# Optimization experiments

Measured on AMD Instinct MI355X. Metric: run time of the kernel, lower is better.

The kernel has to match this reference:

```python
import jax, jax.numpy as jnp
import numpy as np
import math

B, S, D, H, FF, NB = 32, 512, 512, 8, 2048, 2
DK = D // H  # 64
NEG = -1e30  # stands in for torch's -1e32 (fp32-safe)


def _make_pe():
    # CosinePositionalEmbedding: deterministic sin/cos part (the 0.1*randn is fully overwritten)
    pos = np.arange(S, dtype=np.float32)[:, None]
    div = np.exp(np.arange(0, D, 2, dtype=np.float32) * -(math.log(10000.0) / D))
    pe = np.zeros((S, D), np.float32)
    pe[:, 0::2] = np.sin(pos * div)
    pe[:, 1::2] = np.cos(pos * div)
    return jnp.asarray(pe)[None]  # [1, S, D]


def setup_inputs() -> dict:
    key = jax.random.key(0)
    ks = jax.random.split(key, 10)
    def w(k, shape):
        return jax.random.normal(k, shape, jnp.float32) * 0.02
    return {
        "q_embed_data": jax.random.normal(ks[0], (B, S, D), jnp.float32),
        "qa_embed_data": jax.random.normal(ks[1], (B, S, D), jnp.float32),
        "forget_rate": jax.random.uniform(ks[2], (B, 1, S, 1), jnp.float32),
        "pe": _make_pe(),
        "Wk": w(ks[3], (NB, D, D)), "bk": jnp.zeros((NB, D), jnp.float32),
        "Wv": w(ks[4], (NB, D, D)), "bv": jnp.zeros((NB, D), jnp.float32),
        "Wo": w(ks[5], (NB, D, D)), "bo": jnp.zeros((NB, D), jnp.float32),
        "g1": jnp.ones((NB, D), jnp.float32), "be1": jnp.zeros((NB, D), jnp.float32),
        "W1": w(ks[6], (NB, D, FF)), "bf1": jnp.zeros((NB, FF), jnp.float32),
        "W2": w(ks[7], (NB, FF, D)), "bf2": jnp.zeros((NB, D), jnp.float32),
        "g2": jnp.ones((NB, D), jnp.float32), "be2": jnp.zeros((NB, D), jnp.float32),
    }


def _ln(x, g, b):
    m = jnp.mean(x, axis=-1, keepdims=True)
    v = jnp.var(x, axis=-1, keepdims=True)
    return (x - m) * jax.lax.rsqrt(v + 1e-5) * g + b


def reference(q_embed_data, qa_embed_data, forget_rate, pe, Wk, bk, Wv, bv, Wo, bo,
              g1, be1, W1, bf1, W2, bf2, g2, be2):
    x = q_embed_data + pe[:, :S]   # query stream
    y = qa_embed_data + pe[:, :S]  # value stream (constant across blocks)
    # mask==0 path: src_mask True where triu(k=0)==0, i.e. strictly-past positions j < i
    allowed = jnp.tril(jnp.ones((S, S), bool), k=-1)
    scale = 1.0 / math.sqrt(DK)
    for i in range(NB):
        # kq_same=True: q and k both use k_linear; query=key=x so q == k
        q = (x @ Wk[i] + bk[i]).reshape(B, S, H, DK).transpose(0, 2, 1, 3)  # [B,H,S,dk]
        k = q
        v = (y @ Wv[i] + bv[i]).reshape(B, S, H, DK).transpose(0, 2, 1, 3)
        scores = jnp.einsum('bhqd,bhkd->bhqk', q, k) * scale      # [B,H,S,S]
        scores = scores * forget_rate                              # broadcast [B,1,S,1]
        scores = jnp.where(allowed, scores, NEG)                   # masked_fill(mask==0, -1e32)
        attn = jax.nn.softmax(scores, axis=-1)
        attn = attn.at[:, :, 0, :].set(0.0)                        # zero_pad first query row
        out = jnp.einsum('bhqk,bhkd->bhqd', attn, v)
        out = out.transpose(0, 2, 1, 3).reshape(B, S, D) @ Wo[i] + bo[i]
        x = _ln(x + out, g1[i], be1[i])
        ffn = jax.nn.relu(x @ W1[i] + bf1[i]) @ W2[i] + bf2[i]
        x = _ln(x + ffn, g2[i], be2[i])
    return x
```

## Files before the change

### kernel.cpp

```cpp
#include <hip/hip_runtime.h>

#define B_ 32
#define S_ 512
#define D_ 512
#define H_ 8
#define DK_ 64
#define FF_ 2048

typedef float f32x4 __attribute__((ext_vector_type(4)));
typedef __bf16 bf16x8 __attribute__((ext_vector_type(8)));
typedef __bf16 bf16x4 __attribute__((ext_vector_type(4)));

__device__ __forceinline__ void gld_lds16(const void* gptr, void* lptr) {
    auto g = (__attribute__((address_space(1))) void*)(unsigned long long)gptr;
    auto l = (__attribute__((address_space(3))) void*)(unsigned)(unsigned long long)lptr;
    __builtin_amdgcn_global_load_lds(g, l, 16, 0, 0);
}

__global__ __launch_bounds__(256) void prep_kernel(
    const float* __restrict__ q, const float* __restrict__ qa,
    const float* __restrict__ pe, __bf16* __restrict__ xbf,
    __bf16* __restrict__ ybf)
{
    const int n4 = B_ * S_ * D_ / 4;
    for (int i = blockIdx.x * blockDim.x + threadIdx.x; i < n4;
         i += gridDim.x * blockDim.x) {
        float4 pv = ((const float4*)pe)[i & (S_ * D_ / 4 - 1)];
        float4 qv = ((const float4*)q)[i];
        float4 av = ((const float4*)qa)[i];
        bf16x4 xb = {(__bf16)(qv.x + pv.x), (__bf16)(qv.y + pv.y),
                     (__bf16)(qv.z + pv.z), (__bf16)(qv.w + pv.w)};
        ((bf16x4*)xbf)[i] = xb;
        bf16x4 yb = {(__bf16)(av.x + pv.x), (__bf16)(av.y + pv.y),
                     (__bf16)(av.z + pv.z), (__bf16)(av.w + pv.w)};
        ((bf16x4*)ybf)[i] = yb;
    }
}

__device__ __forceinline__ void ttile(
    const float* __restrict__ in, __bf16* __restrict__ out,
    int R, int C, int bx, int by, int t)
{
    __shared__ float tile[32][33];
    const int tc = bx * 32, tr = by * 32;
    const int lx = t & 31, ly = t >> 5;
    #pragma unroll
    for (int yy = ly; yy < 32; yy += 8)
        tile[yy][lx] = in[(long)(tr + yy) * C + tc + lx];
    __syncthreads();
    #pragma unroll
    for (int yy = ly; yy < 32; yy += 8)
        out[(long)(tc + yy) * R + tr + lx] = (__bf16)tile[lx][yy];
}

__global__ __launch_bounds__(256) void transpose6(
    const float* __restrict__ Wk, const float* __restrict__ Wv,
    const float* __restrict__ Wo, __bf16* __restrict__ ok,
    __bf16* __restrict__ ov, __bf16* __restrict__ oo)
{
    const int z = blockIdx.z, sel = z >> 1, i = z & 1;
    const float* src = sel == 0 ? Wk : (sel == 1 ? Wv : Wo);
    __bf16* dst = sel == 0 ? ok : (sel == 1 ? ov : oo);
    ttile(src + (long)i * 262144, dst + (long)i * 262144, 512, 512,
          blockIdx.x, blockIdx.y, threadIdx.x);
}

__global__ __launch_bounds__(256) void transposeW1(
    const float* __restrict__ W1, __bf16* __restrict__ o1)
{
    const int i = blockIdx.z;
    ttile(W1 + (long)i * 1048576, o1 + (long)i * 1048576, 512, 2048,
          blockIdx.x, blockIdx.y, threadIdx.x);
}

__global__ __launch_bounds__(256) void transposeW2(
    const float* __restrict__ W2, __bf16* __restrict__ o2)
{
    const int i = blockIdx.z;
    ttile(W2 + (long)i * 1048576, o2 + (long)i * 1048576, 2048, 512,
          blockIdx.x, blockIdx.y, threadIdx.x);
}

template <int RELU, int MODE>
__global__ __launch_bounds__(256) void gemm_kernel(
    const __bf16* __restrict__ A, const __bf16* __restrict__ Bt,
    const float* __restrict__ bias, const __bf16* __restrict__ res,
    __bf16* __restrict__ out, int M, int N, int K)
{
    __shared__ __bf16 As[2][128 * 64];
    __shared__ __bf16 Bs[2][128 * 64];
    const int t = threadIdx.x;
    const int lane = t & 63;
    const int wv = t >> 6, wr = wv >> 1, wc = wv & 1;
    const int lr = lane & 15, lk = lane >> 4;

    const int nwg = gridDim.x * gridDim.y;
    const int lin = blockIdx.y * gridDim.x + blockIdx.x;
    const int swz = (lin & 7) * (nwg >> 3) + (lin >> 3);
    const int m0 = (swz / gridDim.x) * 128, n0 = (swz % gridDim.x) * 128;

    const int srow = t >> 3;
    const int sslot = (t & 7) ^ (srow & 7);
    const __bf16* gA = A + (long)(m0 + srow) * K + sslot * 8;
    const __bf16* gB = Bt + (long)(n0 + srow) * K + sslot * 8;
    const long rstep = (long)32 * K;

    auto STAGE = [&](int bsel, int k0) {
        char* ldsA = (char*)As[bsel] + t * 16;
        char* ldsB = (char*)Bs[bsel] + t * 16;
        #pragma unroll
        for (int u = 0; u < 4; ++u) {
            gld_lds16(gA + u * rstep + k0, ldsA + u * 4096);
            gld_lds16(gB + u * rstep + k0, ldsB + u * 4096);
        }
    };

    f32x4 acc[4][4] = {};
    auto COMPUTE = [&](int bsel) {
        #pragma unroll
        for (int kk = 0; kk < 2; ++kk) {
            bf16x8 af[4], bfr[4];
            #pragma unroll
            for (int i = 0; i < 4; ++i) {
                const int rr = wr * 64 + i * 16 + lr;
                af[i] = *(const bf16x8*)((const char*)As[bsel] +
                        (rr << 7) + (((kk * 4 + lk) ^ (rr & 7)) << 4));
            }
            #pragma unroll
            for (int j = 0; j < 4; ++j) {
                const int rr = wc * 64 + j * 16 + lr;
                bfr[j] = *(const bf16x8*)((const char*)Bs[bsel] +
                         (rr << 7) + (((kk * 4 + lk) ^ (rr & 7)) << 4));
            }
            #pragma unroll
            for (int i = 0; i < 4; ++i)
                #pragma unroll
                for (int j = 0; j < 4; ++j)
                    acc[i][j] = __builtin_amdgcn_mfma_f32_16x16x32_bf16(
                        af[i], bfr[j], acc[i][j], 0, 0, 0);
        }
    };

    const int NT = K >> 6;
    STAGE(0, 0);
    STAGE(1, 64);
    for (int kt = 0; kt < NT - 1; ++kt) {
        asm volatile("s_waitcnt vmcnt(8)" ::: "memory");
        __builtin_amdgcn_s_barrier();
        COMPUTE(kt & 1);
        __builtin_amdgcn_s_barrier();
        if (kt + 2 < NT) STAGE(kt & 1, (kt + 2) << 6);
    }
    asm volatile("s_waitcnt vmcnt(0)" ::: "memory");
    __builtin_amdgcn_s_barrier();
    COMPUTE((NT - 1) & 1);

    #pragma unroll
    for (int i = 0; i < 4; ++i) {
        #pragma unroll
        for (int j = 0; j < 4; ++j) {
            const int n = n0 + wc * 64 + j * 16 + lr;
            const float bv = bias[n];
            if (MODE == 2) {
                const int mb = m0 + wr * 64 + i * 16 + lk * 4;
                const int b = mb >> 9, s = mb & 511;
                bf16x4 ov = {(__bf16)(acc[i][j][0] + bv),
                             (__bf16)(acc[i][j][1] + bv),
                             (__bf16)(acc[i][j][2] + bv),
                             (__bf16)(acc[i][j][3] + bv)};
                *(bf16x4*)(out + (((long)(b * 8 + (n >> 6)) * 64 + (n & 63)) << 9) + s) = ov;
            } else {
                #pragma unroll
                for (int r = 0; r < 4; ++r) {
                    const int m = m0 + wr * 64 + i * 16 + lk * 4 + r;
                    const long off = (long)m * N + n;
                    float v = acc[i][j][r] + bv;
                    if (MODE == 1) v += (float)res[off];
                    if (RELU) v = v > 0.f ? v : 0.f;
                    out[off] = (__bf16)v;
                }
            }
        }
    }
}

__global__ __launch_bounds__(256) void attn_kernel(
    const __bf16* __restrict__ Q, const __bf16* __restrict__ Vt,
    const float* __restrict__ fr, __bf16* __restrict__ Out)
{
    __shared__ __bf16 Ks[64 * 64];
    __shared__ __bf16 Vs[64 * 64];
    __shared__ __bf16 Plds[4][16 * 64];
    const int t = threadIdx.x;
    const int lane = t & 63, wv = t >> 6;
    const int lr = lane & 15, lk = lane >> 4;
    const int qb = blockIdx.x, h = blockIdx.y, b = blockIdx.z;
    const int qT = qb * 64 + wv * 16;

    const __bf16* qp = Q + (long)(b * S_ + qT + lr) * D_ + h * DK_ + lk * 8;
    const bf16x8 qf0 = *(const bf16x8*)qp;
    const bf16x8 qf1 = *(const bf16x8*)(qp + 32);

    float frv[4], ls[4];
    #pragma unroll
    for (int r = 0; r < 4; ++r) {
        frv[r] = fr[b * S_ + qT + lk * 4 + r] * 0.125f;
        ls[r] = 0.f;
    }
    f32x4 o[4] = {};

    const int srow = t >> 3;
    const int sslot = (t & 7) ^ (srow & 7);
    const __bf16* kstage = Q + (long)(b * S_ + srow) * D_ + h * DK_ + sslot * 8;
    const __bf16* vstage = Vt + ((long)(b * H_ + h) * DK_ + srow) * S_ + sslot * 8;
    char* kd = (char*)Ks + t * 16;
    char* vd = (char*)Vs + t * 16;
    __bf16* pl = &Plds[wv][0];
    const int sw = (lr & 7);

    for (int ks = 0; ks <= qb * 64; ks += 64) {
        gld_lds16(kstage + (long)ks * D_, kd);
        gld_lds16(kstage + (long)(ks + 32) * D_, kd + 4096);
        gld_lds16(vstage + ks, vd);
        gld_lds16(vstage + ks + 32 * S_, vd + 4096);
        __syncthreads();

        f32x4 s[4] = {};
        #pragma unroll
        for (int j = 0; j < 4; ++j) {
            const char* kb = (const char*)Ks + ((j * 16 + lr) << 7);
            const bf16x8 kf0 = *(const bf16x8*)(kb + ((lk ^ sw) << 4));
            const bf16x8 kf1 = *(const bf16x8*)(kb + (((lk + 4) ^ sw) << 4));
            s[j] = __builtin_amdgcn_mfma_f32_16x16x32_bf16(qf0, kf0, s[j], 0, 0, 0);
            s[j] = __builtin_amdgcn_mfma_f32_16x16x32_bf16(qf1, kf1, s[j], 0, 0, 0);
        }
        #pragma unroll
        for (int j = 0; j < 4; ++j) {
            const int col = ks + j * 16 + lr;
            const int c8 = j * 2 + (lr >> 3), cb = lr & 7;
            #pragma unroll
            for (int r = 0; r < 4; ++r) {
                const int row = lk * 4 + r;
                const int sidx = row * 64 + ((c8 ^ (row & 7)) << 3) + cb;
                const float e = __expf(s[j][r] * frv[r]);
                const float p = (col < qT + row) ? e : 0.f;
                ls[r] += p;
                pl[sidx] = (__bf16)p;
            }
        }
        bf16x8 pf[2];
        #pragma unroll
        for (int kk = 0; kk < 2; ++kk) {
            const int ridx = lr * 64 + (((kk * 4 + lk) ^ sw) << 3);
            pf[kk] = *(const bf16x8*)&pl[ridx];
        }
        #pragma unroll
        for (int dt = 0; dt < 4; ++dt) {
            const char* vb = (const char*)Vs + ((dt * 16 + lr) << 7);
            #pragma unroll
            for (int kk = 0; kk < 2; ++kk) {
                const bf16x8 vf = *(const bf16x8*)(vb + (((kk * 4 + lk) ^ sw) << 4));
                o[dt] = __builtin_amdgcn_mfma_f32_16x16x32_bf16(pf[kk], vf, o[dt], 0, 0, 0);
            }
        }
        __syncthreads();
    }

    #pragma unroll
    for (int r = 0; r < 4; ++r) {
        #pragma unroll
        for (int d = 1; d < 16; d <<= 1)
            ls[r] += __shfl_xor(ls[r], d);
        const float inv = ls[r] > 0.f ? 1.f / ls[r] : 0.f;
        #pragma unroll
        for (int dt = 0; dt < 4; ++dt)
            Out[(long)(b * S_ + qT + lk * 4 + r) * D_ + h * DK_ + dt * 16 + lr] =
                (__bf16)(o[dt][r] * inv);
    }
}

__global__ __launch_bounds__(256) void ln_kernel(
    const __bf16* __restrict__ pre, const float* __restrict__ g,
    const float* __restrict__ be, float* __restrict__ xout,
    __bf16* __restrict__ xbf, int wf32)
{
    const int lane = threadIdx.x & 63, wv = threadIdx.x >> 6;
    const long row = (long)blockIdx.x * 4 + wv;
    const bf16x8 v = *(const bf16x8*)(pre + row * D_ + lane * 8);
    float f[8];
    #pragma unroll
    for (int k = 0; k < 8; ++k) f[k] = (float)v[k];
    float s = 0.f, ss = 0.f;
    #pragma unroll
    for (int k = 0; k < 8; ++k) { s += f[k]; ss += f[k] * f[k]; }
    #pragma unroll
    for (int d = 1; d < 64; d <<= 1) {
        s  += __shfl_xor(s, d);
        ss += __shfl_xor(ss, d);
    }
    const float mean = s * (1.f / 512.f);
    const float rstd = rsqrtf(ss * (1.f / 512.f) - mean * mean + 1e-5f);
    const float4 ga = ((const float4*)(g + lane * 8))[0];
    const float4 gc = ((const float4*)(g + lane * 8))[1];
    const float4 ba = ((const float4*)(be + lane * 8))[0];
    const float4 bc = ((const float4*)(be + lane * 8))[1];
    float o[8];
    o[0] = (f[0] - mean) * rstd * ga.x + ba.x;
    o[1] = (f[1] - mean) * rstd * ga.y + ba.y;
    o[2] = (f[2] - mean) * rstd * ga.z + ba.z;
    o[3] = (f[3] - mean) * rstd * ga.w + ba.w;
    o[4] = (f[4] - mean) * rstd * gc.x + bc.x;
    o[5] = (f[5] - mean) * rstd * gc.y + bc.y;
    o[6] = (f[6] - mean) * rstd * gc.z + bc.z;
    o[7] = (f[7] - mean) * rstd * gc.w + bc.w;
    bf16x8 xb = {(__bf16)o[0], (__bf16)o[1], (__bf16)o[2], (__bf16)o[3],
                 (__bf16)o[4], (__bf16)o[5], (__bf16)o[6], (__bf16)o[7]};
    *(bf16x8*)(xbf + row * D_ + lane * 8) = xb;
    if (wf32) {
        float* xo = xout + row * D_ + lane * 8;
        ((float4*)xo)[0] = make_float4(o[0], o[1], o[2], o[3]);
        ((float4*)xo)[1] = make_float4(o[4], o[5], o[6], o[7]);
    }
}

extern "C" void kernel_launch(void* const* d_in, const int* in_sizes, int n_in,
                              void* d_out, int out_size, void* d_ws, size_t ws_size,
                              hipStream_t stream) {
    const float* q_embed = (const float*)d_in[0];
    const float* qa_embed = (const float*)d_in[1];
    const float* fr  = (const float*)d_in[2];
    const float* pe  = (const float*)d_in[3];
    const float* Wk  = (const float*)d_in[4];
    const float* bk  = (const float*)d_in[5];
    const float* Wv  = (const float*)d_in[6];
    const float* bv  = (const float*)d_in[7];
    const float* Wo  = (const float*)d_in[8];
    const float* bo  = (const float*)d_in[9];
    const float* g1  = (const float*)d_in[10];
    const float* be1 = (const float*)d_in[11];
    const float* W1  = (const float*)d_in[12];
    const float* bf1 = (const float*)d_in[13];
    const float* W2  = (const float*)d_in[14];
    const float* bf2 = (const float*)d_in[15];
    const float* g2  = (const float*)d_in[16];
    const float* be2 = (const float*)d_in[17];

    char* ws = (char*)d_ws;
    __bf16* xbf   = (__bf16*)(ws + 0);
    __bf16* ybf   = (__bf16*)(ws + 16777216);
    __bf16* pool  = (__bf16*)(ws + 33554432);
    __bf16* preln = (__bf16*)(ws + 100663296);
    __bf16* wts   = (__bf16*)(ws + 117440512);

    __bf16* kbuf  = pool;
    __bf16* vtbuf = pool + 8388608;
    __bf16* abuf  = pool + 2 * 8388608;
    __bf16* f1buf = pool;

    __bf16* wkt = wts;
    __bf16* wvt = wts + 524288;
    __bf16* wot = wts + 1048576;
    __bf16* w1t = wts + 1572864;
    __bf16* w2t = wts + 3670016;

    transpose6 <<<dim3(16, 16, 6), 256, 0, stream>>>(Wk, Wv, Wo, wkt, wvt, wot);
    transposeW1<<<dim3(64, 16, 2), 256, 0, stream>>>(W1, w1t);
    transposeW2<<<dim3(16, 64, 2), 256, 0, stream>>>(W2, w2t);
    prep_kernel<<<2048, 256, 0, stream>>>(q_embed, qa_embed, pe, xbf, ybf);

    for (int i = 0; i < 2; ++i) {
        gemm_kernel<0, 0><<<dim3(4, 128), 256, 0, stream>>>(
            xbf, wkt + i * 262144, bk + i * 512, nullptr, kbuf, 16384, 512, 512);
        gemm_kernel<0, 2><<<dim3(4, 128), 256, 0, stream>>>(
            ybf, wvt + i * 262144, bv + i * 512, nullptr, vtbuf, 16384, 512, 512);
        attn_kernel<<<dim3(8, 8, 32), 256, 0, stream>>>(kbuf, vtbuf, fr, abuf);
        gemm_kernel<0, 1><<<dim3(4, 128), 256, 0, stream>>>(
            abuf, wot + i * 262144, bo + i * 512, xbf, preln, 16384, 512, 512);
        ln_kernel<<<4096, 256, 0, stream>>>(preln, g1 + i * 512, be1 + i * 512,
                                            (float*)d_out, xbf, 0);
        gemm_kernel<1, 0><<<dim3(16, 128), 256, 0, stream>>>(
            xbf, w1t + i * 1048576, bf1 + i * 2048, nullptr, f1buf, 16384, 2048, 512);
        gemm_kernel<0, 1><<<dim3(4, 128), 256, 0, stream>>>(
            f1buf, w2t + i * 1048576, bf2 + i * 512, xbf, preln, 16384, 512, 2048);
        ln_kernel<<<4096, 256, 0, stream>>>(preln, g2 + i * 512, be2 + i * 512,
                                            (float*)d_out, xbf, i == 1 ? 1 : 0);
    }
}
```

Measured before the change: 447.9 us.

## Double-buffer attention K/V tiles, batch K/V GEMMs, merge weight transposes

The attention kernel now double-buffers its K and V LDS tiles, prefetching the next key block while it computes the current one, in place of a load-then-sync per iteration. The K and V projection GEMMs are merged into one launch using a z-dimension selector, which doubles the grid so the work fills the GPU better. The three weight-transpose kernels become a single launch. In exchange, attention LDS use doubles, which may lower occupancy.

```diff
diff --git a/kernel.cpp b/kernel.cpp
--- a/kernel.cpp
+++ b/kernel.cpp
@@ -53,32 +53,30 @@
         out[(long)(tc + yy) * R + tr + lx] = (__bf16)tile[lx][yy];
 }
 
-__global__ __launch_bounds__(256) void transpose6(
+__global__ __launch_bounds__(256) void transpose_all(
     const float* __restrict__ Wk, const float* __restrict__ Wv,
-    const float* __restrict__ Wo, __bf16* __restrict__ ok,
-    __bf16* __restrict__ ov, __bf16* __restrict__ oo)
-{
-    const int z = blockIdx.z, sel = z >> 1, i = z & 1;
-    const float* src = sel == 0 ? Wk : (sel == 1 ? Wv : Wo);
-    __bf16* dst = sel == 0 ? ok : (sel == 1 ? ov : oo);
-    ttile(src + (long)i * 262144, dst + (long)i * 262144, 512, 512,
-          blockIdx.x, blockIdx.y, threadIdx.x);
-}
-
-__global__ __launch_bounds__(256) void transposeW1(
-    const float* __restrict__ W1, __bf16* __restrict__ o1)
-{
-    const int i = blockIdx.z;
-    ttile(W1 + (long)i * 1048576, o1 + (long)i * 1048576, 512, 2048,
-          blockIdx.x, blockIdx.y, threadIdx.x);
-}
-
-__global__ __launch_bounds__(256) void transposeW2(
-    const float* __restrict__ W2, __bf16* __restrict__ o2)
-{
-    const int i = blockIdx.z;
-    ttile(W2 + (long)i * 1048576, o2 + (long)i * 1048576, 2048, 512,
-          blockIdx.x, blockIdx.y, threadIdx.x);
+    const float* __restrict__ Wo, const float* __restrict__ W1,
+    const float* __restrict__ W2, __bf16* __restrict__ ok,
+    __bf16* __restrict__ ov, __bf16* __restrict__ oo,
+    __bf16* __restrict__ o1, __bf16* __restrict__ o2)
+{
+    const int id = blockIdx.x, t = threadIdx.x;
+    if (id < 1536) {
+        const int z = id >> 8, r = id & 255;
+        const int sel = z >> 1, i = z & 1;
+        const float* src = sel == 0 ? Wk : (sel == 1 ? Wv : Wo);
+        __bf16* dst = sel == 0 ? ok : (sel == 1 ? ov : oo);
+        ttile(src + (long)i * 262144, dst + (long)i * 262144, 512, 512,
+              r & 15, r >> 4, t);
+    } else if (id < 3584) {
+        int r = id - 1536; const int i = r >> 10; r &= 1023;
+        ttile(W1 + (long)i * 1048576, o1 + (long)i * 1048576, 512, 2048,
+              r & 63, r >> 6, t);
+    } else {
+        int r = id - 3584; const int i = r >> 10; r &= 1023;
+        ttile(W2 + (long)i * 1048576, o2 + (long)i * 1048576, 2048, 512,
+              r & 15, r >> 4, t);
+    }
 }
 
 template <int RELU, int MODE>
@@ -161,23 +159,119 @@
         for (int j = 0; j < 4; ++j) {
             const int n = n0 + wc * 64 + j * 16 + lr;
             const float bv = bias[n];
-            if (MODE == 2) {
+            #pragma unroll
+            for (int r = 0; r < 4; ++r) {
+                const int m = m0 + wr * 64 + i * 16 + lk * 4 + r;
+                const long off = (long)m * N + n;
+                float v = acc[i][j][r] + bv;
+                if (MODE == 1) v += (float)res[off];
+                if (RELU) v = v > 0.f ? v : 0.f;
+                out[off] = (__bf16)v;
+            }
+        }
+    }
+}
+
+__global__ __launch_bounds__(256) void gemm_kv(
+    const __bf16* __restrict__ xbf, const __bf16* __restrict__ ybf,
+    const __bf16* __restrict__ wkt, const __bf16* __restrict__ wvt,
+    const float* __restrict__ bk, const float* __restrict__ bv,
+    __bf16* __restrict__ kout, __bf16* __restrict__ vtout)
+{
+    constexpr int N = 512, K = 512;
+    __shared__ __bf16 As[2][128 * 64];
+    __shared__ __bf16 Bs[2][128 * 64];
+    const int t = threadIdx.x;
+    const int lane = t & 63;
+    const int wv = t >> 6, wr = wv >> 1, wc = wv & 1;
+    const int lr = lane & 15, lk = lane >> 4;
+    const int zv = blockIdx.z;
+
+    const __bf16* A  = zv ? ybf : xbf;
+    const __bf16* Bt = zv ? wvt : wkt;
+    const float* bias = zv ? bv : bk;
+    __bf16* out = zv ? vtout : kout;
+
+    const int nwg = gridDim.x * gridDim.y;
+    const int lin = blockIdx.y * gridDim.x + blockIdx.x;
+    const int swz = (lin & 7) * (nwg >> 3) + (lin >> 3);
+    const int m0 = (swz / gridDim.x) * 128, n0 = (swz % gridDim.x) * 128;
+
+    const int srow = t >> 3;
+    const int sslot = (t & 7) ^ (srow & 7);
+    const __bf16* gA = A + (long)(m0 + srow) * K + sslot * 8;
+    const __bf16* gB = Bt + (long)(n0 + srow) * K + sslot * 8;
+    const long rstep = (long)32 * K;
+
+    auto STAGE = [&](int bsel, int k0) {
+        char* ldsA = (char*)As[bsel] + t * 16;
+        char* ldsB = (char*)Bs[bsel] + t * 16;
+        #pragma unroll
+        for (int u = 0; u < 4; ++u) {
+            gld_lds16(gA + u * rstep + k0, ldsA + u * 4096);
+            gld_lds16(gB + u * rstep + k0, ldsB + u * 4096);
+        }
+    };
+
+    f32x4 acc[4][4] = {};
+    auto COMPUTE = [&](int bsel) {
+        #pragma unroll
+        for (int kk = 0; kk < 2; ++kk) {
+            bf16x8 af[4], bfr[4];
+            #pragma unroll
+            for (int i = 0; i < 4; ++i) {
+                const int rr = wr * 64 + i * 16 + lr;
+                af[i] = *(const bf16x8*)((const char*)As[bsel] +
+                        (rr << 7) + (((kk * 4 + lk) ^ (rr & 7)) << 4));
+            }
+            #pragma unroll
+            for (int j = 0; j < 4; ++j) {
+                const int rr = wc * 64 + j * 16 + lr;
+                bfr[j] = *(const bf16x8*)((const char*)Bs[bsel] +
+                         (rr << 7) + (((kk * 4 + lk) ^ (rr & 7)) << 4));
+            }
+            #pragma unroll
+            for (int i = 0; i < 4; ++i)
+                #pragma unroll
+                for (int j = 0; j < 4; ++j)
+                    acc[i][j] = __builtin_amdgcn_mfma_f32_16x16x32_bf16(
+                        af[i], bfr[j], acc[i][j], 0, 0, 0);
+        }
+    };
+
+    const int NT = K >> 6;
+    STAGE(0, 0);
+    STAGE(1, 64);
+    for (int kt = 0; kt < NT - 1; ++kt) {
+        asm volatile("s_waitcnt vmcnt(8)" ::: "memory");
+        __builtin_amdgcn_s_barrier();
+        COMPUTE(kt & 1);
+        __builtin_amdgcn_s_barrier();
+        if (kt + 2 < NT) STAGE(kt & 1, (kt + 2) << 6);
+    }
+    asm volatile("s_waitcnt vmcnt(0)" ::: "memory");
+    __builtin_amdgcn_s_barrier();
+    COMPUTE((NT - 1) & 1);
+
+    #pragma unroll
+    for (int i = 0; i < 4; ++i) {
+        #pragma unroll
+        for (int j = 0; j < 4; ++j) {
+            const int n = n0 + wc * 64 + j * 16 + lr;
+            const float bvl = bias[n];
+            if (zv) {
                 const int mb = m0 + wr * 64 + i * 16 + lk * 4;
                 const int b = mb >> 9, s = mb & 511;
-                bf16x4 ov = {(__bf16)(acc[i][j][0] + bv),
-                             (__bf16)(acc[i][j][1] + bv),
-                             (__bf16)(acc[i][j][2] + bv),
-                             (__bf16)(acc[i][j][3] + bv)};
+                bf16x4 ov = {(__bf16)(acc[i][j][0] + bvl),
+                             (__bf16)(acc[i][j][1] + bvl),
+                             (__bf16)(acc[i][j][2] + bvl),
+                             (__bf16)(acc[i][j][3] + bvl)};
                 *(bf16x4*)(out + (((long)(b * 8 + (n >> 6)) * 64 + (n & 63)) << 9) + s) = ov;
             } else {
                 #pragma unroll
                 for (int r = 0; r < 4; ++r) {
                     const int m = m0 + wr * 64 + i * 16 + lk * 4 + r;
-                    const long off = (long)m * N + n;
-                    float v = acc[i][j][r] + bv;
-                    if (MODE == 1) v += (float)res[off];
-                    if (RELU) v = v > 0.f ? v : 0.f;
-                    out[off] = (__bf16)v;
+                    out[(long)m * N + n] = (__bf16)(acc[i][j][r] + bvl);
                 }
             }
         }
@@ -188,8 +282,8 @@
     const __bf16* __restrict__ Q, const __bf16* __restrict__ Vt,
     const float* __restrict__ fr, __bf16* __restrict__ Out)
 {
-    __shared__ __bf16 Ks[64 * 64];
-    __shared__ __bf16 Vs[64 * 64];
+    __shared__ __bf16 Ks[2][64 * 64];
+    __shared__ __bf16 Vs[2][64 * 64];
     __shared__ __bf16 Plds[4][16 * 64];
     const int t = threadIdx.x;
     const int lane = t & 63, wv = t >> 6;
@@ -213,26 +307,25 @@
     const int sslot = (t & 7) ^ (srow & 7);
     const __bf16* kstage = Q + (long)(b * S_ + srow) * D_ + h * DK_ + sslot * 8;
     const __bf16* vstage = Vt + ((long)(b * H_ + h) * DK_ + srow) * S_ + sslot * 8;
-    char* kd = (char*)Ks + t * 16;
-    char* vd = (char*)Vs + t * 16;
     __bf16* pl = &Plds[wv][0];
     const int sw = (lr & 7);
 
-    for (int ks = 0; ks <= qb * 64; ks += 64) {
-        gld_lds16(kstage + (long)ks * D_, kd);
-        gld_lds16(kstage + (long)(ks + 32) * D_, kd + 4096);
-        gld_lds16(vstage + ks, vd);
-        gld_lds16(vstage + ks + 32 * S_, vd + 4096);
-        __syncthreads();
-
-        f32x4 s[4] = {};
+    auto STAGE = [&](int bsel, int ks) {
+        gld_lds16(kstage + (long)ks * D_, (char*)Ks[bsel] + t * 16);
+        gld_lds16(kstage + (long)(ks + 32) * D_, (char*)Ks[bsel] + 4096 + t * 16);
+        gld_lds16(vstage + ks, (char*)Vs[bsel] + t * 16);
+        gld_lds16(vstage + ks + 32 * S_, (char*)Vs[bsel] + 4096 + t * 16);
+    };
+
+    auto COMPUTE = [&](int bsel, int ks) {
+        f32x4 sc[4] = {};
         #pragma unroll
         for (int j = 0; j < 4; ++j) {
-            const char* kb = (const char*)Ks + ((j * 16 + lr) << 7);
+            const char* kb = (const char*)Ks[bsel] + ((j * 16 + lr) << 7);
             const bf16x8 kf0 = *(const bf16x8*)(kb + ((lk ^ sw) << 4));
             const bf16x8 kf1 = *(const bf16x8*)(kb + (((lk + 4) ^ sw) << 4));
-            s[j] = __builtin_amdgcn_mfma_f32_16x16x32_bf16(qf0, kf0, s[j], 0, 0, 0);
-            s[j] = __builtin_amdgcn_mfma_f32_16x16x32_bf16(qf1, kf1, s[j], 0, 0, 0);
+            sc[j] = __builtin_amdgcn_mfma_f32_16x16x32_bf16(qf0, kf0, sc[j], 0, 0, 0);
+            sc[j] = __builtin_amdgcn_mfma_f32_16x16x32_bf16(qf1, kf1, sc[j], 0, 0, 0);
         }
         #pragma unroll
         for (int j = 0; j < 4; ++j) {
@@ -242,7 +335,7 @@
             for (int r = 0; r < 4; ++r) {
                 const int row = lk * 4 + r;
                 const int sidx = row * 64 + ((c8 ^ (row & 7)) << 3) + cb;
-                const float e = __expf(s[j][r] * frv[r]);
+                const float e = __expf(sc[j][r] * frv[r]);
                 const float p = (col < qT + row) ? e : 0.f;
                 ls[r] += p;
                 pl[sidx] = (__bf16)p;
@@ -256,15 +349,28 @@
         }
         #pragma unroll
         for (int dt = 0; dt < 4; ++dt) {
-            const char* vb = (const char*)Vs + ((dt * 16 + lr) << 7);
+            const char* vb = (const char*)Vs[bsel] + ((dt * 16 + lr) << 7);
             #pragma unroll
             for (int kk = 0; kk < 2; ++kk) {
                 const bf16x8 vf = *(const bf16x8*)(vb + (((kk * 4 + lk) ^ sw) << 4));
                 o[dt] = __builtin_amdgcn_mfma_f32_16x16x32_bf16(pf[kk], vf, o[dt], 0, 0, 0);
             }
         }
-        __syncthreads();
-    }
+    };
+
+    const int nt = qb + 1;
+    STAGE(0, 0);
+    if (nt > 1) STAGE(1, 64);
+    for (int tt = 0; tt < nt - 1; ++tt) {
+        asm volatile("s_waitcnt vmcnt(4)" ::: "memory");
+        __builtin_amdgcn_s_barrier();
+        COMPUTE(tt & 1, tt * 64);
+        __builtin_amdgcn_s_barrier();
+        if (tt + 2 < nt) STAGE(tt & 1, (tt + 2) * 64);
+    }
+    asm volatile("s_waitcnt vmcnt(0)" ::: "memory");
+    __builtin_amdgcn_s_barrier();
+    COMPUTE((nt - 1) & 1, (nt - 1) * 64);
 
     #pragma unroll
     for (int r = 0; r < 4; ++r) {
@@ -363,16 +469,14 @@
     __bf16* w1t = wts + 1572864;
     __bf16* w2t = wts + 3670016;
 
-    transpose6 <<<dim3(16, 16, 6), 256, 0, stream>>>(Wk, Wv, Wo, wkt, wvt, wot);
-    transposeW1<<<dim3(64, 16, 2), 256, 0, stream>>>(W1, w1t);
-    transposeW2<<<dim3(16, 64, 2), 256, 0, stream>>>(W2, w2t);
+    transpose_all<<<5632, 256, 0, stream>>>(Wk, Wv, Wo, W1, W2,
+                                            wkt, wvt, wot, w1t, w2t);
     prep_kernel<<<2048, 256, 0, stream>>>(q_embed, qa_embed, pe, xbf, ybf);
 
     for (int i = 0; i < 2; ++i) {
-        gemm_kernel<0, 0><<<dim3(4, 128), 256, 0, stream>>>(
-            xbf, wkt + i * 262144, bk + i * 512, nullptr, kbuf, 16384, 512, 512);
-        gemm_kernel<0, 2><<<dim3(4, 128), 256, 0, stream>>>(
-            ybf, wvt + i * 262144, bv + i * 512, nullptr, vtbuf, 16384, 512, 512);
+        gemm_kv<<<dim3(4, 128, 2), 256, 0, stream>>>(
+            xbf, ybf, wkt + i * 262144, wvt + i * 262144,
+            bk + i * 512, bv + i * 512, kbuf, vtbuf);
         attn_kernel<<<dim3(8, 8, 32), 256, 0, stream>>>(kbuf, vtbuf, fr, abuf);
         gemm_kernel<0, 1><<<dim3(4, 128), 256, 0, stream>>>(
             abuf, wot + i * 262144, bo + i * 512, xbf, preln, 16384, 512, 512);
```

After: 438.0 us. -2.2%, faster.
